# Performance work log

Measured on AMD Instinct MI355X. Metric: run time of the kernel, lower is better.

Reference implementation:

```python
import jax, jax.numpy as jnp
import numpy as np

B, A, F = 8192, 8, 256      # batch, n_agents, per-agent obs feature dim
NA = 16                     # n_actions per agent
H1, H2 = 1024, 1024
OBS_D = A * F               # 2048 flattened obs dim
ACT_D = A * NA              # 128 joint action dim
IN_D = OBS_D + ACT_D        # 2176 MLP input dim


def setup_inputs() -> dict:
    key = jax.random.key(0)
    ks = jax.random.split(key, 8)
    s = 0.02
    return {
        "obs": jax.random.normal(ks[0], (B, A, F), dtype=jnp.float32),
        "all_actions": jax.random.uniform(ks[1], (B, ACT_D), dtype=jnp.float32),
        # per-agent stacked MLP params (agent axis first)
        "W1": jax.random.normal(ks[2], (A, IN_D, H1), dtype=jnp.float32) * s,
        "b1": jnp.zeros((A, H1), dtype=jnp.float32),
        "W2": jax.random.normal(ks[3], (A, H1, H2), dtype=jnp.float32) * s,
        "b2": jnp.zeros((A, H2), dtype=jnp.float32),
        "W3": jax.random.normal(ks[4], (A, H2, NA), dtype=jnp.float32) * s,
        "b3": jnp.zeros((A, NA), dtype=jnp.float32),
    }


def reference(obs, all_actions, W1, b1, W2, b2, W3, b3):
    b_s = obs.shape[0]
    obs_flat = obs.reshape(b_s, OBS_D)                      # [B, A*F]
    # mask[a, g] = 0 on agent a's own action block, 1 elsewhere
    mask = 1.0 - jnp.repeat(jnp.eye(A, dtype=obs.dtype), NA, axis=1)  # [A, A*NA]
    # split W1 into obs / action columns (equivalent to concat-then-dense)
    W1o = W1[:, :OBS_D, :]                                  # [A, OBS_D, H1]
    W1a = W1[:, OBS_D:, :]                                  # [A, ACT_D, H1]
    h1 = jax.nn.relu(
        jnp.einsum("bd,adh->bah", obs_flat, W1o)
        + jnp.einsum("bg,ag,agh->bah", all_actions, mask, W1a)
        + b1
    )                                                        # [B, A, H1]
    h2 = jax.nn.relu(jnp.einsum("bah,ahk->bak", h1, W2) + b2)  # [B, A, H2]
    out = jnp.einsum("bak,akn->ban", h2, W3) + b3              # [B, A, NA]
    return out.reshape(b_s, A * NA)
```

## Files before the change

### kernel.cpp

```cpp
#include <hip/hip_runtime.h>
#include <hip/hip_bf16.h>
#include <cstdint>
#include <cstddef>

typedef __bf16 bf16;
typedef __attribute__((ext_vector_type(8))) __bf16 bf16x8;
typedef __attribute__((ext_vector_type(4))) float f32x4;
typedef __attribute__((ext_vector_type(4))) int i32x4;
typedef __attribute__((address_space(3))) const bf16* lds_cp;

#define B_SZ  8192
#define NAGENT 8
#define NA_N  16
#define OBS_DD 2048
#define ACT_DD 128
#define IN_DD 2176
#define H1_D  1024
#define H2_D  1024

#define BM 256
#define BN 256
#define BK 64
#define GRID_M (B_SZ / BM)
#define GRID_N (1024 / BN)

__device__ __forceinline__ void gload16(const void* g, void* l) {
    __builtin_amdgcn_global_load_lds(
        (__attribute__((address_space(1))) void*)(g),
        (__attribute__((address_space(3))) void*)(l), 16, 0, 0);
}


__global__ void k_convert_x(const float* __restrict__ obs,
                            const float* __restrict__ act,
                            bf16* __restrict__ xb) {
    const int chunks = IN_DD / 8;
    int idx = blockIdx.x * blockDim.x + threadIdx.x;
    if (idx >= B_SZ * chunks) return;
    int b = idx / chunks;
    int c8 = idx - b * chunks;
    const float* src = (c8 < OBS_DD / 8)
        ? (obs + (size_t)b * OBS_DD + c8 * 8)
        : (act + (size_t)b * ACT_DD + (c8 - OBS_DD / 8) * 8);
    float4 v0 = ((const float4*)src)[0];
    float4 v1 = ((const float4*)src)[1];
    bf16x8 o;
    o[0] = (bf16)v0.x; o[1] = (bf16)v0.y; o[2] = (bf16)v0.z; o[3] = (bf16)v0.w;
    o[4] = (bf16)v1.x; o[5] = (bf16)v1.y; o[6] = (bf16)v1.z; o[7] = (bf16)v1.w;
    ((bf16x8*)(xb + (size_t)b * IN_DD))[c8] = o;
}

__global__ void k_transpose_w(const float* __restrict__ src, bf16* __restrict__ dst,
                              int K, int H, int maskStart) {
    __shared__ float tile[32][33];
    int a = blockIdx.z;
    int k0 = blockIdx.x * 32, h0 = blockIdx.y * 32;
    const float* s = src + (size_t)a * K * H;
    bf16* d = dst + (size_t)a * K * H;
    int tx = threadIdx.x, ty = threadIdx.y;
    #pragma unroll
    for (int i = 0; i < 32; i += 8) {
        int k = k0 + ty + i;
        float v = s[(size_t)k * H + h0 + tx];
        if (k >= maskStart) {
            int g = k - maskStart;
            if ((g >> 4) == a) v = 0.f;
        }
        tile[ty + i][tx] = v;
    }
    __syncthreads();
    #pragma unroll
    for (int i = 0; i < 32; i += 8) {
        d[(size_t)(h0 + ty + i) * K + k0 + tx] = (bf16)tile[tx][ty + i];
    }
}

__global__ void k_transpose_w3(const float* __restrict__ src, bf16* __restrict__ dst) {
    int idx = blockIdx.x * blockDim.x + threadIdx.x;
    if (idx >= NAGENT * NA_N * H2_D) return;
    int a = idx / (NA_N * H2_D);
    int n = (idx / H2_D) % NA_N;
    int k = idx % H2_D;
    dst[idx] = (bf16)src[(size_t)a * H2_D * NA_N + (size_t)k * NA_N + n];
}

__global__ void k_init_out(const float* __restrict__ b3, float* __restrict__ out) {
    int i = blockIdx.x * blockDim.x + threadIdx.x;
    if (i < B_SZ * NAGENT * NA_N) out[i] = b3[i & 127];
}

#define DSR4(d0, d1, d2, d3, addr, O0, O1, O2, O3)                      \
    asm volatile("ds_read_b128 %0, %4 offset:" #O0 "\n\t"               \
                 "ds_read_b128 %1, %4 offset:" #O1 "\n\t"               \
                 "ds_read_b128 %2, %4 offset:" #O2 "\n\t"               \
                 "ds_read_b128 %3, %4 offset:" #O3                      \
                 : "=&v"(d0), "=&v"(d1), "=&v"(d2), "=&v"(d3)           \
                 : "v"(addr))

#define BC(x) __builtin_bit_cast(bf16x8, x)

template<int FUSE>
__global__ __launch_bounds__(512, 1)
void k_gemm256(const bf16* __restrict__ Ain, size_t aStride, int lda,
               const bf16* __restrict__ Bw, const float* __restrict__ bias,
               bf16* __restrict__ Cout, size_t cStride, int K,
               int aOff, int gridZ,
               const bf16* __restrict__ W3Tp, float* __restrict__ outp) {
    extern __shared__ bf16 lds[];

    const int tid = threadIdx.x;
    const int w = tid >> 6;
    const int l = tid & 63;

    int flat = blockIdx.x + GRID_M * (blockIdx.y + GRID_N * blockIdx.z);
    int q8 = (GRID_M * GRID_N * gridZ) >> 3;
    int lin2 = (flat & 7) * q8 + (flat >> 3);
    const int mt = lin2 % GRID_M;
    int rest = lin2 / GRID_M;
    const int ntile = rest % GRID_N;
    const int az = rest / GRID_N;
    const int aw = az + aOff;

    const int rowBase = mt * BM;
    const int colBase = ntile * BN;
    const bf16* Aag = Ain + (size_t)az * aStride;
    const bf16* Bag = Bw + (size_t)aw * (size_t)1024 * K;

    const int wr = (w >> 2) * 128;
    const int wc = (w & 3) * 64;
    const int lr = l & 15;
    const int lq = l >> 4;

    const int rowA = (wr + lr) * BK;
    const int rowB = (wc + lr) * BK;
    const int ck0 = ((lq ^ (lr & 7)) * 8);
    const int ck1 = (((4 + lq) ^ (lr & 7)) * 8);

    const int sRow = w * 16 + (l >> 3);
    const int sCol = ((l & 7) ^ (l >> 3)) * 8;
    const bf16* pA0 = Aag + (size_t)(rowBase + sRow) * lda + sCol;
    const bf16* pA1 = Aag + (size_t)(rowBase + 128 + sRow) * lda + sCol;
    const bf16* pB0 = Bag + (size_t)(colBase + sRow) * K + sCol;
    const bf16* pB1 = Bag + (size_t)(colBase + 128 + sRow) * K + sCol;
    const size_t l8a = (size_t)8 * lda;
    const size_t l8b = (size_t)8 * K;

    const int nkt = K / BK;

#define STAGE_A(t1, half) do {                                              \
        const bf16* g_ = ((half) ? pA1 : pA0) + (t1) * BK;                  \
        bf16* d_ = &lds[(((t1) & 1) * 16384) + (half) * 8192 + w * 1024];   \
        gload16(g_, d_);                                                    \
        gload16(g_ + l8a, d_ + 512);                                        \
    } while (0)
#define STAGE_B(t2, half) do {                                              \
        const bf16* g_ = ((half) ? pB1 : pB0) + (t2) * BK;                  \
        bf16* d_ = &lds[32768 + (((t2) & 1) * 16384) + (half) * 8192 + w * 1024]; \
        gload16(g_, d_);                                                    \
        gload16(g_ + l8b, d_ + 512);                                        \
    } while (0)

    f32x4 acc[8][4] = {};
    i32x4 ra0, ra1, ra2, ra3;
    i32x4 rb0, rb1, rb2, rb3;
    i32x4 rc0, rc1, rc2, rc3;
    i32x4 rd0, rd1, rd2, rd3;
    i32x4 re0, re1, re2, re3;
    i32x4 rf0, rf1, rf2, rf3;

#define MFMA16(ACC0, A0, A1, A2, A3, B0, B1, B2, B3)                        \
    do {                                                                    \
        acc[ACC0+0][0] = __builtin_amdgcn_mfma_f32_16x16x32_bf16(BC(A0), BC(B0), acc[ACC0+0][0], 0, 0, 0); \
        acc[ACC0+1][0] = __builtin_amdgcn_mfma_f32_16x16x32_bf16(BC(A1), BC(B0), acc[ACC0+1][0], 0, 0, 0); \
        acc[ACC0+2][0] = __builtin_amdgcn_mfma_f32_16x16x32_bf16(BC(A2), BC(B0), acc[ACC0+2][0], 0, 0, 0); \
        acc[ACC0+3][0] = __builtin_amdgcn_mfma_f32_16x16x32_bf16(BC(A3), BC(B0), acc[ACC0+3][0], 0, 0, 0); \
        acc[ACC0+0][1] = __builtin_amdgcn_mfma_f32_16x16x32_bf16(BC(A0), BC(B1), acc[ACC0+0][1], 0, 0, 0); \
        acc[ACC0+1][1] = __builtin_amdgcn_mfma_f32_16x16x32_bf16(BC(A1), BC(B1), acc[ACC0+1][1], 0, 0, 0); \
        acc[ACC0+2][1] = __builtin_amdgcn_mfma_f32_16x16x32_bf16(BC(A2), BC(B1), acc[ACC0+2][1], 0, 0, 0); \
        acc[ACC0+3][1] = __builtin_amdgcn_mfma_f32_16x16x32_bf16(BC(A3), BC(B1), acc[ACC0+3][1], 0, 0, 0); \
        acc[ACC0+0][2] = __builtin_amdgcn_mfma_f32_16x16x32_bf16(BC(A0), BC(B2), acc[ACC0+0][2], 0, 0, 0); \
        acc[ACC0+1][2] = __builtin_amdgcn_mfma_f32_16x16x32_bf16(BC(A1), BC(B2), acc[ACC0+1][2], 0, 0, 0); \
        acc[ACC0+2][2] = __builtin_amdgcn_mfma_f32_16x16x32_bf16(BC(A2), BC(B2), acc[ACC0+2][2], 0, 0, 0); \
        acc[ACC0+3][2] = __builtin_amdgcn_mfma_f32_16x16x32_bf16(BC(A3), BC(B2), acc[ACC0+3][2], 0, 0, 0); \
        acc[ACC0+0][3] = __builtin_amdgcn_mfma_f32_16x16x32_bf16(BC(A0), BC(B3), acc[ACC0+0][3], 0, 0, 0); \
        acc[ACC0+1][3] = __builtin_amdgcn_mfma_f32_16x16x32_bf16(BC(A1), BC(B3), acc[ACC0+1][3], 0, 0, 0); \
        acc[ACC0+2][3] = __builtin_amdgcn_mfma_f32_16x16x32_bf16(BC(A2), BC(B3), acc[ACC0+2][3], 0, 0, 0); \
        acc[ACC0+3][3] = __builtin_amdgcn_mfma_f32_16x16x32_bf16(BC(A3), BC(B3), acc[ACC0+3][3], 0, 0, 0); \
    } while (0)

    STAGE_A(0, 0); STAGE_A(0, 1);
    STAGE_B(0, 0); STAGE_B(0, 1);
    asm volatile("s_waitcnt vmcnt(0)" ::: "memory");
    __builtin_amdgcn_s_barrier();

    for (int t = 0; t < nkt; ++t) {
        const int dbuf = (t & 1) * 16384;
        lds_cp adrA0 = (lds_cp)lds + (dbuf + rowA + ck0);
        lds_cp adrA1 = (lds_cp)lds + (dbuf + rowA + ck1);
        lds_cp adrB0 = (lds_cp)lds + (32768 + dbuf + rowB + ck0);
        lds_cp adrB1 = (lds_cp)lds + (32768 + dbuf + rowB + ck1);

        DSR4(ra0, ra1, ra2, ra3, adrA0, 0, 2048, 4096, 6144);
        DSR4(rb0, rb1, rb2, rb3, adrB0, 0, 2048, 4096, 6144);
        DSR4(rc0, rc1, rc2, rc3, adrA0, 8192, 10240, 12288, 14336);
        DSR4(rd0, rd1, rd2, rd3, adrB1, 0, 2048, 4096, 6144);

        if (t + 1 < nkt) {
            STAGE_A(t + 1, 0); STAGE_A(t + 1, 1);
            STAGE_B(t + 1, 0); STAGE_B(t + 1, 1);
        }

        asm volatile("s_waitcnt lgkmcnt(8)" ::: "memory");
        __builtin_amdgcn_sched_barrier(0);
        __builtin_amdgcn_s_setprio(1);
        MFMA16(0, ra0, ra1, ra2, ra3, rb0, rb1, rb2, rb3);
        __builtin_amdgcn_s_setprio(0);

        DSR4(re0, re1, re2, re3, adrA1, 0, 2048, 4096, 6144);
        asm volatile("s_waitcnt lgkmcnt(4)" ::: "memory");
        __builtin_amdgcn_sched_barrier(0);
        __builtin_amdgcn_s_setprio(1);
        MFMA16(4, rc0, rc1, rc2, rc3, rb0, rb1, rb2, rb3);
        __builtin_amdgcn_s_setprio(0);

        DSR4(rf0, rf1, rf2, rf3, adrA1, 8192, 10240, 12288, 14336);
        asm volatile("s_waitcnt lgkmcnt(4)" ::: "memory");
        __builtin_amdgcn_sched_barrier(0);
        __builtin_amdgcn_s_setprio(1);
        MFMA16(0, re0, re1, re2, re3, rd0, rd1, rd2, rd3);
        __builtin_amdgcn_s_setprio(0);

        asm volatile("s_waitcnt vmcnt(0)" ::: "memory");
        asm volatile("s_waitcnt lgkmcnt(0)" ::: "memory");
        __builtin_amdgcn_sched_barrier(0);
        __builtin_amdgcn_s_setprio(1);
        MFMA16(4, rf0, rf1, rf2, rf3, rd0, rd1, rd2, rd3);
        __builtin_amdgcn_s_setprio(0);

        __builtin_amdgcn_s_barrier();
    }
#undef STAGE_A
#undef STAGE_B
#undef MFMA16

    __syncthreads();
    const float* bAg = bias + (size_t)aw * 1024;
    float bb4[4];
    #pragma unroll
    for (int n = 0; n < 4; ++n) bb4[n] = bAg[colBase + wc + n * 16 + lr];
    #pragma unroll
    for (int m = 0; m < 8; ++m)
        #pragma unroll
        for (int n = 0; n < 4; ++n)
            #pragma unroll
            for (int r = 0; r < 4; ++r) {
                float v = acc[m][n][r] + bb4[n];
                v = fmaxf(v, 0.f);
                int row = wr + m * 16 + lq * 4 + r;
                int col = wc + n * 16 + lr;
                lds[row * 256 + ((((col >> 3) ^ (row & 7)) << 3) | (col & 7))] = (bf16)v;
            }
    __syncthreads();

    if constexpr (!FUSE) {
        bf16* Cg = Cout + (size_t)az * cStride + (size_t)rowBase * 1024 + colBase;
        const int er = tid >> 5;
        const int ec = tid & 31;
        #pragma unroll
        for (int i = 0; i < 16; ++i) {
            int row = i * 16 + er;
            int phys = ec ^ (row & 7);
            *(bf16x8*)&Cg[(size_t)row * 1024 + ec * 8] =
                *(const bf16x8*)&lds[row * 256 + phys * 8];
        }
    } else {
        const bf16* w3a = W3Tp + (size_t)aw * NA_N * H2_D;
        f32x4 oacc[2] = {};
        const int frow0 = w * 32;
        #pragma unroll
        for (int ks = 0; ks < 8; ++ks) {
            bf16x8 bfrag = *(const bf16x8*)&w3a[(size_t)lr * H2_D + colBase + ks * 32 + lq * 8];
            #pragma unroll
            for (int mm = 0; mm < 2; ++mm) {
                int row = frow0 + mm * 16 + lr;
                int lc = (ks * 4 + lq) ^ (row & 7);
                bf16x8 afrag = *(const bf16x8*)&lds[row * 256 + lc * 8];
                oacc[mm] = __builtin_amdgcn_mfma_f32_16x16x32_bf16(afrag, bfrag, oacc[mm], 0, 0, 0);
            }
        }
        #pragma unroll
        for (int mm = 0; mm < 2; ++mm)
            #pragma unroll
            for (int r = 0; r < 4; ++r)
                atomicAdd(&outp[(size_t)(rowBase + frow0 + mm * 16 + lq * 4 + r) * 128
                                + aw * NA_N + lr], oacc[mm][r]);
    }
}

extern "C" void kernel_launch(void* const* d_in, const int* in_sizes, int n_in,
                              void* d_out, int out_size, void* d_ws, size_t ws_size,
                              hipStream_t stream) {
    const float* obs = (const float*)d_in[0];
    const float* act = (const float*)d_in[1];
    const float* W1 = (const float*)d_in[2];
    const float* b1 = (const float*)d_in[3];
    const float* W2 = (const float*)d_in[4];
    const float* b2 = (const float*)d_in[5];
    const float* W3 = (const float*)d_in[6];
    const float* b3 = (const float*)d_in[7];
    float* out = (float*)d_out;

    const size_t SZ_XB  = (size_t)B_SZ * IN_DD * 2;
    const size_t SZ_W1T = (size_t)NAGENT * H1_D * IN_DD * 2;
    const size_t SZ_W2T = (size_t)NAGENT * H1_D * H2_D * 2;
    const size_t SZ_W3T = (size_t)NAGENT * NA_N * H2_D * 2;
    const size_t SZ_H1  = (size_t)B_SZ * H1_D * 2;
    const size_t SZ_FIX = SZ_XB + SZ_W1T + SZ_W2T + SZ_W3T;

    char* ws = (char*)d_ws;
    bf16* Xb  = (bf16*)ws;
    bf16* W1T = (bf16*)(ws + SZ_XB);
    bf16* W2T = (bf16*)(ws + SZ_XB + SZ_W1T);
    bf16* W3T = (bf16*)(ws + SZ_XB + SZ_W1T + SZ_W2T);
    char* hbase = ws + SZ_FIX;

    int G = 8;
    while (G > 1 && ws_size < SZ_FIX + (size_t)G * SZ_H1) G >>= 1;

    (void)hipFuncSetAttribute((const void*)k_gemm256<0>,
                              hipFuncAttributeMaxDynamicSharedMemorySize, 131072);
    (void)hipFuncSetAttribute((const void*)k_gemm256<1>,
                              hipFuncAttributeMaxDynamicSharedMemorySize, 131072);

    k_init_out<<<(B_SZ * 128 + 255) / 256, 256, 0, stream>>>(b3, out);

    {
        int n = B_SZ * (IN_DD / 8);
        k_convert_x<<<(n + 255) / 256, 256, 0, stream>>>(obs, act, Xb);
    }
    k_transpose_w<<<dim3(IN_DD / 32, H1_D / 32, NAGENT), dim3(32, 8), 0, stream>>>(
        W1, W1T, IN_DD, H1_D, OBS_DD);
    k_transpose_w<<<dim3(H1_D / 32, H2_D / 32, NAGENT), dim3(32, 8), 0, stream>>>(
        W2, W2T, H1_D, H2_D, 1 << 30);
    {
        int n = NAGENT * NA_N * H2_D;
        k_transpose_w3<<<(n + 255) / 256, 256, 0, stream>>>(W3, W3T);
    }

    const size_t agElems = (size_t)B_SZ * H1_D;
    bf16* h1 = (bf16*)hbase;

    for (int g0 = 0; g0 < NAGENT; g0 += G) {
        k_gemm256<0><<<dim3(GRID_M, GRID_N, G), 512, 131072, stream>>>(
            Xb, 0, IN_DD, W1T, b1, h1, agElems, IN_DD, g0, G, nullptr, nullptr);
        k_gemm256<1><<<dim3(GRID_M, GRID_N, G), 512, 131072, stream>>>(
            h1, agElems, H1_D, W2T, b2, nullptr, 0, H1_D, g0, G, W3T, out);
    }
    (void)in_sizes; (void)n_in; (void)out_size;
}
```

Before: 455.1 us.

## Switch 256x256 GEMM to 4 waves with 128x128 per-wave tiles

Halves the GEMM workgroup to 256 threads, with each wave now computing a 128x128 output sub-tile (8x8 MFMA accumulators) instead of 128x64. Global-to-LDS staging is reorganised so that waves 0-1 load A and waves 2-3 load B, 16 rows-of-8 each. The LDS fragment reads and MFMA phases are reordered to suit the larger tile, and the vmcnt wait moves to the end of the iteration. The aim is to raise MFMA work per LDS read and cut wave count, at the cost of much higher VGPR/AGPR pressure (256 accumulator floats) and fewer waves to hide latency.

```diff
diff --git a/kernel.cpp b/kernel.cpp
--- a/kernel.cpp
+++ b/kernel.cpp
@@ -100,7 +100,7 @@
 #define BC(x) __builtin_bit_cast(bf16x8, x)
 
 template<int FUSE>
-__global__ __launch_bounds__(512, 1)
+__global__ __launch_bounds__(256, 1)
 void k_gemm256(const bf16* __restrict__ Ain, size_t aStride, int lda,
                const bf16* __restrict__ Bw, const float* __restrict__ bias,
                bf16* __restrict__ Cout, size_t cStride, int K,
@@ -126,70 +126,48 @@
     const bf16* Aag = Ain + (size_t)az * aStride;
     const bf16* Bag = Bw + (size_t)aw * (size_t)1024 * K;
 
-    const int wr = (w >> 2) * 128;
-    const int wc = (w & 3) * 64;
+    const int wrq = (w >> 1) * 128;
+    const int wcq = (w & 1) * 128;
     const int lr = l & 15;
     const int lq = l >> 4;
 
-    const int rowA = (wr + lr) * BK;
-    const int rowB = (wc + lr) * BK;
+    const int rowA = (wrq + lr) * BK;
+    const int rowB = (wcq + lr) * BK;
     const int ck0 = ((lq ^ (lr & 7)) * 8);
     const int ck1 = (((4 + lq) ^ (lr & 7)) * 8);
 
-    const int sRow = w * 16 + (l >> 3);
     const int sCol = ((l & 7) ^ (l >> 3)) * 8;
-    const bf16* pA0 = Aag + (size_t)(rowBase + sRow) * lda + sCol;
-    const bf16* pA1 = Aag + (size_t)(rowBase + 128 + sRow) * lda + sCol;
-    const bf16* pB0 = Bag + (size_t)(colBase + sRow) * K + sCol;
-    const bf16* pB1 = Bag + (size_t)(colBase + 128 + sRow) * K + sCol;
-    const size_t l8a = (size_t)8 * lda;
-    const size_t l8b = (size_t)8 * K;
+    const size_t ldS = (w & 2) ? (size_t)K : (size_t)lda;
+    const bf16* pS = (w & 2)
+        ? (Bag + (size_t)(colBase + (w & 1) * 128 + (l >> 3)) * K + sCol)
+        : (Aag + (size_t)(rowBase + (w & 1) * 128 + (l >> 3)) * lda + sCol);
+    const int sBase = ((w & 2) ? 32768 : 0) + (w & 1) * 8192;
 
     const int nkt = K / BK;
 
-#define STAGE_A(t1, half) do {                                              \
-        const bf16* g_ = ((half) ? pA1 : pA0) + (t1) * BK;                  \
-        bf16* d_ = &lds[(((t1) & 1) * 16384) + (half) * 8192 + w * 1024];   \
-        gload16(g_, d_);                                                    \
-        gload16(g_ + l8a, d_ + 512);                                        \
+#define STAGE(t1) do {                                                      \
+        const bf16* g_ = pS + (size_t)(t1) * BK;                            \
+        bf16* d_ = &lds[(((t1) & 1) * 16384) + sBase];                      \
+        _Pragma("unroll")                                                   \
+        for (int j_ = 0; j_ < 16; ++j_)                                     \
+            gload16(g_ + (size_t)j_ * 8 * ldS, d_ + j_ * 512);              \
     } while (0)
-#define STAGE_B(t2, half) do {                                              \
-        const bf16* g_ = ((half) ? pB1 : pB0) + (t2) * BK;                  \
-        bf16* d_ = &lds[32768 + (((t2) & 1) * 16384) + (half) * 8192 + w * 1024]; \
-        gload16(g_, d_);                                                    \
-        gload16(g_ + l8b, d_ + 512);                                        \
+
+    f32x4 acc[8][8] = {};
+    i32x4 fa[8], fb[8];
+    i32x4 fe[8], ff[8];
+
+#define MFMA_BLK(AF, BF, N0)                                                \
+    do {                                                                    \
+        _Pragma("unroll")                                                   \
+        for (int n_ = 0; n_ < 4; ++n_)                                      \
+            _Pragma("unroll")                                               \
+            for (int m_ = 0; m_ < 8; ++m_)                                  \
+                acc[m_][N0 + n_] = __builtin_amdgcn_mfma_f32_16x16x32_bf16( \
+                    BC(AF[m_]), BC(BF[N0 + n_]), acc[m_][N0 + n_], 0, 0, 0);\
     } while (0)
 
-    f32x4 acc[8][4] = {};
-    i32x4 ra0, ra1, ra2, ra3;
-    i32x4 rb0, rb1, rb2, rb3;
-    i32x4 rc0, rc1, rc2, rc3;
-    i32x4 rd0, rd1, rd2, rd3;
-    i32x4 re0, re1, re2, re3;
-    i32x4 rf0, rf1, rf2, rf3;
-
-#define MFMA16(ACC0, A0, A1, A2, A3, B0, B1, B2, B3)                        \
-    do {                                                                    \
-        acc[ACC0+0][0] = __builtin_amdgcn_mfma_f32_16x16x32_bf16(BC(A0), BC(B0), acc[ACC0+0][0], 0, 0, 0); \
-        acc[ACC0+1][0] = __builtin_amdgcn_mfma_f32_16x16x32_bf16(BC(A1), BC(B0), acc[ACC0+1][0], 0, 0, 0); \
-        acc[ACC0+2][0] = __builtin_amdgcn_mfma_f32_16x16x32_bf16(BC(A2), BC(B0), acc[ACC0+2][0], 0, 0, 0); \
-        acc[ACC0+3][0] = __builtin_amdgcn_mfma_f32_16x16x32_bf16(BC(A3), BC(B0), acc[ACC0+3][0], 0, 0, 0); \
-        acc[ACC0+0][1] = __builtin_amdgcn_mfma_f32_16x16x32_bf16(BC(A0), BC(B1), acc[ACC0+0][1], 0, 0, 0); \
-        acc[ACC0+1][1] = __builtin_amdgcn_mfma_f32_16x16x32_bf16(BC(A1), BC(B1), acc[ACC0+1][1], 0, 0, 0); \
-        acc[ACC0+2][1] = __builtin_amdgcn_mfma_f32_16x16x32_bf16(BC(A2), BC(B1), acc[ACC0+2][1], 0, 0, 0); \
-        acc[ACC0+3][1] = __builtin_amdgcn_mfma_f32_16x16x32_bf16(BC(A3), BC(B1), acc[ACC0+3][1], 0, 0, 0); \
-        acc[ACC0+0][2] = __builtin_amdgcn_mfma_f32_16x16x32_bf16(BC(A0), BC(B2), acc[ACC0+0][2], 0, 0, 0); \
-        acc[ACC0+1][2] = __builtin_amdgcn_mfma_f32_16x16x32_bf16(BC(A1), BC(B2), acc[ACC0+1][2], 0, 0, 0); \
-        acc[ACC0+2][2] = __builtin_amdgcn_mfma_f32_16x16x32_bf16(BC(A2), BC(B2), acc[ACC0+2][2], 0, 0, 0); \
-        acc[ACC0+3][2] = __builtin_amdgcn_mfma_f32_16x16x32_bf16(BC(A3), BC(B2), acc[ACC0+3][2], 0, 0, 0); \
-        acc[ACC0+0][3] = __builtin_amdgcn_mfma_f32_16x16x32_bf16(BC(A0), BC(B3), acc[ACC0+0][3], 0, 0, 0); \
-        acc[ACC0+1][3] = __builtin_amdgcn_mfma_f32_16x16x32_bf16(BC(A1), BC(B3), acc[ACC0+1][3], 0, 0, 0); \
-        acc[ACC0+2][3] = __builtin_amdgcn_mfma_f32_16x16x32_bf16(BC(A2), BC(B3), acc[ACC0+2][3], 0, 0, 0); \
-        acc[ACC0+3][3] = __builtin_amdgcn_mfma_f32_16x16x32_bf16(BC(A3), BC(B3), acc[ACC0+3][3], 0, 0, 0); \
-    } while (0)
-
-    STAGE_A(0, 0); STAGE_A(0, 1);
-    STAGE_B(0, 0); STAGE_B(0, 1);
+    STAGE(0);
     asm volatile("s_waitcnt vmcnt(0)" ::: "memory");
     __builtin_amdgcn_s_barrier();
 
@@ -200,64 +178,64 @@
         lds_cp adrB0 = (lds_cp)lds + (32768 + dbuf + rowB + ck0);
         lds_cp adrB1 = (lds_cp)lds + (32768 + dbuf + rowB + ck1);
 
-        DSR4(ra0, ra1, ra2, ra3, adrA0, 0, 2048, 4096, 6144);
-        DSR4(rb0, rb1, rb2, rb3, adrB0, 0, 2048, 4096, 6144);
-        DSR4(rc0, rc1, rc2, rc3, adrA0, 8192, 10240, 12288, 14336);
-        DSR4(rd0, rd1, rd2, rd3, adrB1, 0, 2048, 4096, 6144);
-
-        if (t + 1 < nkt) {
-            STAGE_A(t + 1, 0); STAGE_A(t + 1, 1);
-            STAGE_B(t + 1, 0); STAGE_B(t + 1, 1);
-        }
+        DSR4(fa[0], fa[1], fa[2], fa[3], adrA0, 0, 2048, 4096, 6144);
+        DSR4(fa[4], fa[5], fa[6], fa[7], adrA0, 8192, 10240, 12288, 14336);
+        DSR4(fb[0], fb[1], fb[2], fb[3], adrB0, 0, 2048, 4096, 6144);
+        DSR4(fb[4], fb[5], fb[6], fb[7], adrB0, 8192, 10240, 12288, 14336);
+
+        if (t + 1 < nkt) STAGE(t + 1);
+
+        asm volatile("s_waitcnt lgkmcnt(4)" ::: "memory");
+        __builtin_amdgcn_sched_barrier(0);
+        __builtin_amdgcn_s_setprio(1);
+        MFMA_BLK(fa, fb, 0);
+        __builtin_amdgcn_s_setprio(0);
+
+        DSR4(fe[0], fe[1], fe[2], fe[3], adrA1, 0, 2048, 4096, 6144);
+        DSR4(fe[4], fe[5], fe[6], fe[7], adrA1, 8192, 10240, 12288, 14336);
 
         asm volatile("s_waitcnt lgkmcnt(8)" ::: "memory");
         __builtin_amdgcn_sched_barrier(0);
         __builtin_amdgcn_s_setprio(1);
-        MFMA16(0, ra0, ra1, ra2, ra3, rb0, rb1, rb2, rb3);
+        MFMA_BLK(fa, fb, 4);
         __builtin_amdgcn_s_setprio(0);
 
-        DSR4(re0, re1, re2, re3, adrA1, 0, 2048, 4096, 6144);
+        DSR4(ff[0], ff[1], ff[2], ff[3], adrB1, 0, 2048, 4096, 6144);
+        DSR4(ff[4], ff[5], ff[6], ff[7], adrB1, 8192, 10240, 12288, 14336);
+
         asm volatile("s_waitcnt lgkmcnt(4)" ::: "memory");
         __builtin_amdgcn_sched_barrier(0);
         __builtin_amdgcn_s_setprio(1);
-        MFMA16(4, rc0, rc1, rc2, rc3, rb0, rb1, rb2, rb3);
+        MFMA_BLK(fe, ff, 0);
         __builtin_amdgcn_s_setprio(0);
 
-        DSR4(rf0, rf1, rf2, rf3, adrA1, 8192, 10240, 12288, 14336);
-        asm volatile("s_waitcnt lgkmcnt(4)" ::: "memory");
-        __builtin_amdgcn_sched_barrier(0);
-        __builtin_amdgcn_s_setprio(1);
-        MFMA16(0, re0, re1, re2, re3, rd0, rd1, rd2, rd3);
-        __builtin_amdgcn_s_setprio(0);
-
-        asm volatile("s_waitcnt vmcnt(0)" ::: "memory");
         asm volatile("s_waitcnt lgkmcnt(0)" ::: "memory");
         __builtin_amdgcn_sched_barrier(0);
         __builtin_amdgcn_s_setprio(1);
-        MFMA16(4, rf0, rf1, rf2, rf3, rd0, rd1, rd2, rd3);
+        MFMA_BLK(fe, ff, 4);
         __builtin_amdgcn_s_setprio(0);
 
+        asm volatile("s_waitcnt vmcnt(0)" ::: "memory");
         __builtin_amdgcn_s_barrier();
     }
-#undef STAGE_A
-#undef STAGE_B
-#undef MFMA16
+#undef STAGE
+#undef MFMA_BLK
 
     __syncthreads();
     const float* bAg = bias + (size_t)aw * 1024;
-    float bb4[4];
+    float bb8[8];
     #pragma unroll
-    for (int n = 0; n < 4; ++n) bb4[n] = bAg[colBase + wc + n * 16 + lr];
+    for (int n = 0; n < 8; ++n) bb8[n] = bAg[colBase + wcq + n * 16 + lr];
     #pragma unroll
     for (int m = 0; m < 8; ++m)
         #pragma unroll
-        for (int n = 0; n < 4; ++n)
+        for (int n = 0; n < 8; ++n)
             #pragma unroll
             for (int r = 0; r < 4; ++r) {
-                float v = acc[m][n][r] + bb4[n];
+                float v = acc[m][n][r] + bb8[n];
                 v = fmaxf(v, 0.f);
-                int row = wr + m * 16 + lq * 4 + r;
-                int col = wc + n * 16 + lr;
+                int row = wrq + m * 16 + lq * 4 + r;
+                int col = wcq + n * 16 + lr;
                 lds[row * 256 + ((((col >> 3) ^ (row & 7)) << 3) | (col & 7))] = (bf16)v;
             }
     __syncthreads();
@@ -267,21 +245,21 @@
         const int er = tid >> 5;
         const int ec = tid & 31;
         #pragma unroll
-        for (int i = 0; i < 16; ++i) {
-            int row = i * 16 + er;
+        for (int i = 0; i < 32; ++i) {
+            int row = i * 8 + er;
             int phys = ec ^ (row & 7);
             *(bf16x8*)&Cg[(size_t)row * 1024 + ec * 8] =
                 *(const bf16x8*)&lds[row * 256 + phys * 8];
         }
     } else {
         const bf16* w3a = W3Tp + (size_t)aw * NA_N * H2_D;
-        f32x4 oacc[2] = {};
-        const int frow0 = w * 32;
+        f32x4 oacc[4] = {};
+        const int frow0 = w * 64;
         #pragma unroll
         for (int ks = 0; ks < 8; ++ks) {
             bf16x8 bfrag = *(const bf16x8*)&w3a[(size_t)lr * H2_D + colBase + ks * 32 + lq * 8];
             #pragma unroll
-            for (int mm = 0; mm < 2; ++mm) {
+            for (int mm = 0; mm < 4; ++mm) {
                 int row = frow0 + mm * 16 + lr;
                 int lc = (ks * 4 + lq) ^ (row & 7);
                 bf16x8 afrag = *(const bf16x8*)&lds[row * 256 + lc * 8];
@@ -289,7 +267,7 @@
             }
         }
         #pragma unroll
-        for (int mm = 0; mm < 2; ++mm)
+        for (int mm = 0; mm < 4; ++mm)
             #pragma unroll
             for (int r = 0; r < 4; ++r)
                 atomicAdd(&outp[(size_t)(rowBase + frow0 + mm * 16 + lq * 4 + r) * 128
@@ -351,9 +329,9 @@
     bf16* h1 = (bf16*)hbase;
 
     for (int g0 = 0; g0 < NAGENT; g0 += G) {
-        k_gemm256<0><<<dim3(GRID_M, GRID_N, G), 512, 131072, stream>>>(
+        k_gemm256<0><<<dim3(GRID_M, GRID_N, G), 256, 131072, stream>>>(
             Xb, 0, IN_DD, W1T, b1, h1, agElems, IN_DD, g0, G, nullptr, nullptr);
-        k_gemm256<1><<<dim3(GRID_M, GRID_N, G), 512, 131072, stream>>>(
+        k_gemm256<1><<<dim3(GRID_M, GRID_N, G), 256, 131072, stream>>>(
             h1, agElems, H1_D, W2T, b2, nullptr, 0, H1_D, g0, G, W3T, out);
     }
     (void)in_sizes; (void)n_in; (void)out_size;
```

New measurement: 480.5 us. 5.6% more time.

## Make GEMM kernels persistent and merge small prep kernels into one

Applied to the files above, without the earlier changes.

The GEMM kernels now launch a fixed grid of up to 256 workgroups, one per CU, and each loops over several output tiles using the same XCD-swizzled tile mapping. The aim is to cut per-workgroup launch cost and tail effects. Output init, input conversion and the W3 transpose are merged into a single prep kernel to save launches. The persistent loop adds a sync per tile and cannot overlap one tile's epilogue with the next tile's loads.

```diff
diff --git a/kernel.cpp b/kernel.cpp
--- a/kernel.cpp
+++ b/kernel.cpp
@@ -30,24 +30,39 @@
         (__attribute__((address_space(3))) void*)(l), 16, 0, 0);
 }
 
-
-__global__ void k_convert_x(const float* __restrict__ obs,
-                            const float* __restrict__ act,
-                            bf16* __restrict__ xb) {
-    const int chunks = IN_DD / 8;
+__global__ void k_prep(const float* __restrict__ obs, const float* __restrict__ act,
+                       bf16* __restrict__ xb, const float* __restrict__ b3,
+                       float* __restrict__ out, const float* __restrict__ W3,
+                       bf16* __restrict__ w3t) {
+    const int NX = B_SZ * (IN_DD / 8);
+    const int NO = B_SZ * 128 / 4;
+    const int NW3 = NAGENT * NA_N * H2_D;
     int idx = blockIdx.x * blockDim.x + threadIdx.x;
-    if (idx >= B_SZ * chunks) return;
-    int b = idx / chunks;
-    int c8 = idx - b * chunks;
-    const float* src = (c8 < OBS_DD / 8)
-        ? (obs + (size_t)b * OBS_DD + c8 * 8)
-        : (act + (size_t)b * ACT_DD + (c8 - OBS_DD / 8) * 8);
-    float4 v0 = ((const float4*)src)[0];
-    float4 v1 = ((const float4*)src)[1];
-    bf16x8 o;
-    o[0] = (bf16)v0.x; o[1] = (bf16)v0.y; o[2] = (bf16)v0.z; o[3] = (bf16)v0.w;
-    o[4] = (bf16)v1.x; o[5] = (bf16)v1.y; o[6] = (bf16)v1.z; o[7] = (bf16)v1.w;
-    ((bf16x8*)(xb + (size_t)b * IN_DD))[c8] = o;
+    if (idx < NX) {
+        const int chunks = IN_DD / 8;
+        int b = idx / chunks;
+        int c8 = idx - b * chunks;
+        const float* src = (c8 < OBS_DD / 8)
+            ? (obs + (size_t)b * OBS_DD + c8 * 8)
+            : (act + (size_t)b * ACT_DD + (c8 - OBS_DD / 8) * 8);
+        float4 v0 = ((const float4*)src)[0];
+        float4 v1 = ((const float4*)src)[1];
+        bf16x8 o;
+        o[0] = (bf16)v0.x; o[1] = (bf16)v0.y; o[2] = (bf16)v0.z; o[3] = (bf16)v0.w;
+        o[4] = (bf16)v1.x; o[5] = (bf16)v1.y; o[6] = (bf16)v1.z; o[7] = (bf16)v1.w;
+        ((bf16x8*)(xb + (size_t)b * IN_DD))[c8] = o;
+    } else if (idx < NX + NO) {
+        int i = idx - NX;
+        int c = (i & 31) * 4;
+        float4 v = make_float4(b3[c], b3[c + 1], b3[c + 2], b3[c + 3]);
+        ((float4*)out)[i] = v;
+    } else if (idx < NX + NO + NW3) {
+        int i = idx - NX - NO;
+        int a = i / (NA_N * H2_D);
+        int n = (i / H2_D) % NA_N;
+        int k = i % H2_D;
+        w3t[i] = (bf16)W3[(size_t)a * H2_D * NA_N + (size_t)k * NA_N + n];
+    }
 }
 
 __global__ void k_transpose_w(const float* __restrict__ src, bf16* __restrict__ dst,
@@ -75,20 +90,6 @@
     }
 }
 
-__global__ void k_transpose_w3(const float* __restrict__ src, bf16* __restrict__ dst) {
-    int idx = blockIdx.x * blockDim.x + threadIdx.x;
-    if (idx >= NAGENT * NA_N * H2_D) return;
-    int a = idx / (NA_N * H2_D);
-    int n = (idx / H2_D) % NA_N;
-    int k = idx % H2_D;
-    dst[idx] = (bf16)src[(size_t)a * H2_D * NA_N + (size_t)k * NA_N + n];
-}
-
-__global__ void k_init_out(const float* __restrict__ b3, float* __restrict__ out) {
-    int i = blockIdx.x * blockDim.x + threadIdx.x;
-    if (i < B_SZ * NAGENT * NA_N) out[i] = b3[i & 127];
-}
-
 #define DSR4(d0, d1, d2, d3, addr, O0, O1, O2, O3)                      \
     asm volatile("ds_read_b128 %0, %4 offset:" #O0 "\n\t"               \
                  "ds_read_b128 %1, %4 offset:" #O1 "\n\t"               \
@@ -104,27 +105,13 @@
 void k_gemm256(const bf16* __restrict__ Ain, size_t aStride, int lda,
                const bf16* __restrict__ Bw, const float* __restrict__ bias,
                bf16* __restrict__ Cout, size_t cStride, int K,
-               int aOff, int gridZ,
+               int aOff, int nwg, int iters,
                const bf16* __restrict__ W3Tp, float* __restrict__ outp) {
     extern __shared__ bf16 lds[];
 
     const int tid = threadIdx.x;
     const int w = tid >> 6;
     const int l = tid & 63;
-
-    int flat = blockIdx.x + GRID_M * (blockIdx.y + GRID_N * blockIdx.z);
-    int q8 = (GRID_M * GRID_N * gridZ) >> 3;
-    int lin2 = (flat & 7) * q8 + (flat >> 3);
-    const int mt = lin2 % GRID_M;
-    int rest = lin2 / GRID_M;
-    const int ntile = rest % GRID_N;
-    const int az = rest / GRID_N;
-    const int aw = az + aOff;
-
-    const int rowBase = mt * BM;
-    const int colBase = ntile * BN;
-    const bf16* Aag = Ain + (size_t)az * aStride;
-    const bf16* Bag = Bw + (size_t)aw * (size_t)1024 * K;
 
     const int wr = (w >> 2) * 128;
     const int wc = (w & 3) * 64;
@@ -138,14 +125,18 @@
 
     const int sRow = w * 16 + (l >> 3);
     const int sCol = ((l & 7) ^ (l >> 3)) * 8;
-    const bf16* pA0 = Aag + (size_t)(rowBase + sRow) * lda + sCol;
-    const bf16* pA1 = Aag + (size_t)(rowBase + 128 + sRow) * lda + sCol;
-    const bf16* pB0 = Bag + (size_t)(colBase + sRow) * K + sCol;
-    const bf16* pB1 = Bag + (size_t)(colBase + 128 + sRow) * K + sCol;
     const size_t l8a = (size_t)8 * lda;
     const size_t l8b = (size_t)8 * K;
 
     const int nkt = K / BK;
+    const int q8 = nwg >> 3;
+
+    i32x4 ra0, ra1, ra2, ra3;
+    i32x4 rb0, rb1, rb2, rb3;
+    i32x4 rc0, rc1, rc2, rc3;
+    i32x4 rd0, rd1, rd2, rd3;
+    i32x4 re0, re1, re2, re3;
+    i32x4 rf0, rf1, rf2, rf3;
 
 #define STAGE_A(t1, half) do {                                              \
         const bf16* g_ = ((half) ? pA1 : pA0) + (t1) * BK;                  \
@@ -159,14 +150,6 @@
         gload16(g_, d_);                                                    \
         gload16(g_ + l8b, d_ + 512);                                        \
     } while (0)
-
-    f32x4 acc[8][4] = {};
-    i32x4 ra0, ra1, ra2, ra3;
-    i32x4 rb0, rb1, rb2, rb3;
-    i32x4 rc0, rc1, rc2, rc3;
-    i32x4 rd0, rd1, rd2, rd3;
-    i32x4 re0, re1, re2, re3;
-    i32x4 rf0, rf1, rf2, rf3;
 
 #define MFMA16(ACC0, A0, A1, A2, A3, B0, B1, B2, B3)                        \
     do {                                                                    \
@@ -188,113 +171,137 @@
         acc[ACC0+3][3] = __builtin_amdgcn_mfma_f32_16x16x32_bf16(BC(A3), BC(B3), acc[ACC0+3][3], 0, 0, 0); \
     } while (0)
 
-    STAGE_A(0, 0); STAGE_A(0, 1);
-    STAGE_B(0, 0); STAGE_B(0, 1);
-    asm volatile("s_waitcnt vmcnt(0)" ::: "memory");
-    __builtin_amdgcn_s_barrier();
-
-    for (int t = 0; t < nkt; ++t) {
-        const int dbuf = (t & 1) * 16384;
-        lds_cp adrA0 = (lds_cp)lds + (dbuf + rowA + ck0);
-        lds_cp adrA1 = (lds_cp)lds + (dbuf + rowA + ck1);
-        lds_cp adrB0 = (lds_cp)lds + (32768 + dbuf + rowB + ck0);
-        lds_cp adrB1 = (lds_cp)lds + (32768 + dbuf + rowB + ck1);
-
-        DSR4(ra0, ra1, ra2, ra3, adrA0, 0, 2048, 4096, 6144);
-        DSR4(rb0, rb1, rb2, rb3, adrB0, 0, 2048, 4096, 6144);
-        DSR4(rc0, rc1, rc2, rc3, adrA0, 8192, 10240, 12288, 14336);
-        DSR4(rd0, rd1, rd2, rd3, adrB1, 0, 2048, 4096, 6144);
-
-        if (t + 1 < nkt) {
-            STAGE_A(t + 1, 0); STAGE_A(t + 1, 1);
-            STAGE_B(t + 1, 0); STAGE_B(t + 1, 1);
+    for (int it = 0; it < iters; ++it) {
+        const int b = blockIdx.x + gridDim.x * it;
+        const int lin2 = (b & 7) * q8 + (b >> 3);
+        const int mt = lin2 % GRID_M;
+        const int rest = lin2 / GRID_M;
+        const int ntile = rest % GRID_N;
+        const int az = rest / GRID_N;
+        const int aw = az + aOff;
+
+        const int rowBase = mt * BM;
+        const int colBase = ntile * BN;
+        const bf16* Aag = Ain + (size_t)az * aStride;
+        const bf16* Bag = Bw + (size_t)aw * (size_t)1024 * K;
+
+        const bf16* pA0 = Aag + (size_t)(rowBase + sRow) * lda + sCol;
+        const bf16* pA1 = Aag + (size_t)(rowBase + 128 + sRow) * lda + sCol;
+        const bf16* pB0 = Bag + (size_t)(colBase + sRow) * K + sCol;
+        const bf16* pB1 = Bag + (size_t)(colBase + 128 + sRow) * K + sCol;
+
+        f32x4 acc[8][4] = {};
+
+        STAGE_A(0, 0); STAGE_A(0, 1);
+        STAGE_B(0, 0); STAGE_B(0, 1);
+        asm volatile("s_waitcnt vmcnt(0)" ::: "memory");
+        __builtin_amdgcn_s_barrier();
+
+        for (int t = 0; t < nkt; ++t) {
+            const int dbuf = (t & 1) * 16384;
+            lds_cp adrA0 = (lds_cp)lds + (dbuf + rowA + ck0);
+            lds_cp adrA1 = (lds_cp)lds + (dbuf + rowA + ck1);
+            lds_cp adrB0 = (lds_cp)lds + (32768 + dbuf + rowB + ck0);
+            lds_cp adrB1 = (lds_cp)lds + (32768 + dbuf + rowB + ck1);
+
+            DSR4(ra0, ra1, ra2, ra3, adrA0, 0, 2048, 4096, 6144);
+            DSR4(rb0, rb1, rb2, rb3, adrB0, 0, 2048, 4096, 6144);
+            DSR4(rc0, rc1, rc2, rc3, adrA0, 8192, 10240, 12288, 14336);
+            DSR4(rd0, rd1, rd2, rd3, adrB1, 0, 2048, 4096, 6144);
+
+            if (t + 1 < nkt) {
+                STAGE_A(t + 1, 0); STAGE_A(t + 1, 1);
+                STAGE_B(t + 1, 0); STAGE_B(t + 1, 1);
+            }
+
+            asm volatile("s_waitcnt lgkmcnt(8)" ::: "memory");
+            __builtin_amdgcn_sched_barrier(0);
+            __builtin_amdgcn_s_setprio(1);
+            MFMA16(0, ra0, ra1, ra2, ra3, rb0, rb1, rb2, rb3);
+            __builtin_amdgcn_s_setprio(0);
+
+            DSR4(re0, re1, re2, re3, adrA1, 0, 2048, 4096, 6144);
+            asm volatile("s_waitcnt lgkmcnt(4)" ::: "memory");
+            __builtin_amdgcn_sched_barrier(0);
+            __builtin_amdgcn_s_setprio(1);
+            MFMA16(4, rc0, rc1, rc2, rc3, rb0, rb1, rb2, rb3);
+            __builtin_amdgcn_s_setprio(0);
+
+            DSR4(rf0, rf1, rf2, rf3, adrA1, 8192, 10240, 12288, 14336);
+            asm volatile("s_waitcnt lgkmcnt(4)" ::: "memory");
+            __builtin_amdgcn_sched_barrier(0);
+            __builtin_amdgcn_s_setprio(1);
+            MFMA16(0, re0, re1, re2, re3, rd0, rd1, rd2, rd3);
+            __builtin_amdgcn_s_setprio(0);
+
+            asm volatile("s_waitcnt vmcnt(0)" ::: "memory");
+            asm volatile("s_waitcnt lgkmcnt(0)" ::: "memory");
+            __builtin_amdgcn_sched_barrier(0);
+            __builtin_amdgcn_s_setprio(1);
+            MFMA16(4, rf0, rf1, rf2, rf3, rd0, rd1, rd2, rd3);
+            __builtin_amdgcn_s_setprio(0);
+
+            __builtin_amdgcn_s_barrier();
         }
 
-        asm volatile("s_waitcnt lgkmcnt(8)" ::: "memory");
-        __builtin_amdgcn_sched_barrier(0);
-        __builtin_amdgcn_s_setprio(1);
-        MFMA16(0, ra0, ra1, ra2, ra3, rb0, rb1, rb2, rb3);
-        __builtin_amdgcn_s_setprio(0);
-
-        DSR4(re0, re1, re2, re3, adrA1, 0, 2048, 4096, 6144);
-        asm volatile("s_waitcnt lgkmcnt(4)" ::: "memory");
-        __builtin_amdgcn_sched_barrier(0);
-        __builtin_amdgcn_s_setprio(1);
-        MFMA16(4, rc0, rc1, rc2, rc3, rb0, rb1, rb2, rb3);
-        __builtin_amdgcn_s_setprio(0);
-
-        DSR4(rf0, rf1, rf2, rf3, adrA1, 8192, 10240, 12288, 14336);
-        asm volatile("s_waitcnt lgkmcnt(4)" ::: "memory");
-        __builtin_amdgcn_sched_barrier(0);
-        __builtin_amdgcn_s_setprio(1);
-        MFMA16(0, re0, re1, re2, re3, rd0, rd1, rd2, rd3);
-        __builtin_amdgcn_s_setprio(0);
-
-        asm volatile("s_waitcnt vmcnt(0)" ::: "memory");
-        asm volatile("s_waitcnt lgkmcnt(0)" ::: "memory");
-        __builtin_amdgcn_sched_barrier(0);
-        __builtin_amdgcn_s_setprio(1);
-        MFMA16(4, rf0, rf1, rf2, rf3, rd0, rd1, rd2, rd3);
-        __builtin_amdgcn_s_setprio(0);
-
-        __builtin_amdgcn_s_barrier();
+        __syncthreads();
+        const float* bAg = bias + (size_t)aw * 1024;
+        float bb4[4];
+        #pragma unroll
+        for (int n = 0; n < 4; ++n) bb4[n] = bAg[colBase + wc + n * 16 + lr];
+        #pragma unroll
+        for (int m = 0; m < 8; ++m)
+            #pragma unroll
+            for (int n = 0; n < 4; ++n)
+                #pragma unroll
+                for (int r = 0; r < 4; ++r) {
+                    float v = acc[m][n][r] + bb4[n];
+                    v = fmaxf(v, 0.f);
+                    int row = wr + m * 16 + lq * 4 + r;
+                    int col = wc + n * 16 + lr;
+                    lds[row * 256 + ((((col >> 3) ^ (row & 7)) << 3) | (col & 7))] = (bf16)v;
+                }
+        __syncthreads();
+
+        if constexpr (!FUSE) {
+            bf16* Cg = Cout + (size_t)az * cStride + (size_t)rowBase * 1024 + colBase;
+            const int er = tid >> 5;
+            const int ec = tid & 31;
+            #pragma unroll
+            for (int i = 0; i < 16; ++i) {
+                int row = i * 16 + er;
+                int phys = ec ^ (row & 7);
+                *(bf16x8*)&Cg[(size_t)row * 1024 + ec * 8] =
+                    *(const bf16x8*)&lds[row * 256 + phys * 8];
+            }
+        } else {
+            const bf16* w3a = W3Tp + (size_t)aw * NA_N * H2_D;
+            f32x4 oacc[2] = {};
+            const int frow0 = w * 32;
+            #pragma unroll
+            for (int ks = 0; ks < 8; ++ks) {
+                bf16x8 bfrag = *(const bf16x8*)&w3a[(size_t)lr * H2_D + colBase + ks * 32 + lq * 8];
+                #pragma unroll
+                for (int mm = 0; mm < 2; ++mm) {
+                    int row = frow0 + mm * 16 + lr;
+                    int lc = (ks * 4 + lq) ^ (row & 7);
+                    bf16x8 afrag = *(const bf16x8*)&lds[row * 256 + lc * 8];
+                    oacc[mm] = __builtin_amdgcn_mfma_f32_16x16x32_bf16(afrag, bfrag, oacc[mm], 0, 0, 0);
+                }
+            }
+            #pragma unroll
+            for (int mm = 0; mm < 2; ++mm)
+                #pragma unroll
+                for (int r = 0; r < 4; ++r)
+                    atomicAdd(&outp[(size_t)(rowBase + frow0 + mm * 16 + lq * 4 + r) * 128
+                                    + aw * NA_N + lr], oacc[mm][r]);
+        }
+
+        __syncthreads();
     }
 #undef STAGE_A
 #undef STAGE_B
 #undef MFMA16
-
-    __syncthreads();
-    const float* bAg = bias + (size_t)aw * 1024;
-    float bb4[4];
-    #pragma unroll
-    for (int n = 0; n < 4; ++n) bb4[n] = bAg[colBase + wc + n * 16 + lr];
-    #pragma unroll
-    for (int m = 0; m < 8; ++m)
-        #pragma unroll
-        for (int n = 0; n < 4; ++n)
-            #pragma unroll
-            for (int r = 0; r < 4; ++r) {
-                float v = acc[m][n][r] + bb4[n];
-                v = fmaxf(v, 0.f);
-                int row = wr + m * 16 + lq * 4 + r;
-                int col = wc + n * 16 + lr;
-                lds[row * 256 + ((((col >> 3) ^ (row & 7)) << 3) | (col & 7))] = (bf16)v;
-            }
-    __syncthreads();
-
-    if constexpr (!FUSE) {
-        bf16* Cg = Cout + (size_t)az * cStride + (size_t)rowBase * 1024 + colBase;
-        const int er = tid >> 5;
-        const int ec = tid & 31;
-        #pragma unroll
-        for (int i = 0; i < 16; ++i) {
-            int row = i * 16 + er;
-            int phys = ec ^ (row & 7);
-            *(bf16x8*)&Cg[(size_t)row * 1024 + ec * 8] =
-                *(const bf16x8*)&lds[row * 256 + phys * 8];
-        }
-    } else {
-        const bf16* w3a = W3Tp + (size_t)aw * NA_N * H2_D;
-        f32x4 oacc[2] = {};
-        const int frow0 = w * 32;
-        #pragma unroll
-        for (int ks = 0; ks < 8; ++ks) {
-            bf16x8 bfrag = *(const bf16x8*)&w3a[(size_t)lr * H2_D + colBase + ks * 32 + lq * 8];
-            #pragma unroll
-            for (int mm = 0; mm < 2; ++mm) {
-                int row = frow0 + mm * 16 + lr;
-                int lc = (ks * 4 + lq) ^ (row & 7);
-                bf16x8 afrag = *(const bf16x8*)&lds[row * 256 + lc * 8];
-                oacc[mm] = __builtin_amdgcn_mfma_f32_16x16x32_bf16(afrag, bfrag, oacc[mm], 0, 0, 0);
-            }
-        }
-        #pragma unroll
-        for (int mm = 0; mm < 2; ++mm)
-            #pragma unroll
-            for (int r = 0; r < 4; ++r)
-                atomicAdd(&outp[(size_t)(rowBase + frow0 + mm * 16 + lq * 4 + r) * 128
-                                + aw * NA_N + lr], oacc[mm][r]);
-    }
 }
 
 extern "C" void kernel_launch(void* const* d_in, const int* in_sizes, int n_in,
@@ -332,29 +339,29 @@
     (void)hipFuncSetAttribute((const void*)k_gemm256<1>,
                               hipFuncAttributeMaxDynamicSharedMemorySize, 131072);
 
-    k_init_out<<<(B_SZ * 128 + 255) / 256, 256, 0, stream>>>(b3, out);
-
     {
-        int n = B_SZ * (IN_DD / 8);
-        k_convert_x<<<(n + 255) / 256, 256, 0, stream>>>(obs, act, Xb);
+        const int NX = B_SZ * (IN_DD / 8);
+        const int NO = B_SZ * 128 / 4;
+        const int NW3 = NAGENT * NA_N * H2_D;
+        int n = NX + NO + NW3;
+        k_prep<<<(n + 255) / 256, 256, 0, stream>>>(obs, act, Xb, b3, out, W3, W3T);
     }
     k_transpose_w<<<dim3(IN_DD / 32, H1_D / 32, NAGENT), dim3(32, 8), 0, stream>>>(
         W1, W1T, IN_DD, H1_D, OBS_DD);
     k_transpose_w<<<dim3(H1_D / 32, H2_D / 32, NAGENT), dim3(32, 8), 0, stream>>>(
         W2, W2T, H1_D, H2_D, 1 << 30);
-    {
-        int n = NAGENT * NA_N * H2_D;
-        k_transpose_w3<<<(n + 255) / 256, 256, 0, stream>>>(W3, W3T);
-    }
 
     const size_t agElems = (size_t)B_SZ * H1_D;
     bf16* h1 = (bf16*)hbase;
 
     for (int g0 = 0; g0 < NAGENT; g0 += G) {
-        k_gemm256<0><<<dim3(GRID_M, GRID_N, G), 512, 131072, stream>>>(
-            Xb, 0, IN_DD, W1T, b1, h1, agElems, IN_DD, g0, G, nullptr, nullptr);
-        k_gemm256<1><<<dim3(GRID_M, GRID_N, G), 512, 131072, stream>>>(
-            h1, agElems, H1_D, W2T, b2, nullptr, 0, H1_D, g0, G, W3T, out);
+        const int nwg = 128 * G;
+        const int grd = (nwg >= 256) ? 256 : nwg;
+        const int iters = nwg / grd;
+        k_gemm256<0><<<grd, 512, 131072, stream>>>(
+            Xb, 0, IN_DD, W1T, b1, h1, agElems, IN_DD, g0, nwg, iters, nullptr, nullptr);
+        k_gemm256<1><<<grd, 512, 131072, stream>>>(
+            h1, agElems, H1_D, W2T, b2, nullptr, 0, H1_D, g0, nwg, iters, W3T, out);
     }
     (void)in_sizes; (void)n_in; (void)out_size;
 }
```

Result: slower. 508.2 us (+11.7%).
